# Kernel tuning notes

Hardware: AMD Instinct MI355X
Metric: run time of the kernel (lower is better)

The kernel has to match this reference:

```python
import jax, jax.numpy as jnp
import numpy as np

# ---- static config (matches init_kwargs) ----
R_MAX = 5.0
K_RBF = 32
F = 128            # features_dim
H = 4              # num_att_heads
DH = F // H        # 32
T = 3              # num_interactions
NG = 64            # num_graphs
INV_AVG = 1.0 / 16.0   # 1/avg_num_neighbors
NUM_ELEM = 10
DEG = [1, 3, 5, 7]     # (2l+1) for l=0..3
OFF = np.cumsum([0] + DEG)  # [0,1,4,9,16]
SH = 16

silu = jax.nn.silu


def sph_harm(v):
    """Real spherical harmonics l=0..3, normalized input, e3nn 'component' norm
    (sum_m Y_lm^2 = 2l+1 pointwise). v: [E,3] -> [E,16]."""
    r = jnp.linalg.norm(v, axis=-1, keepdims=True)
    u = v / jnp.maximum(r, 1e-9)
    x, y, z = u[..., 0], u[..., 1], u[..., 2]
    one = jnp.ones_like(x)
    s3, s5, s15 = np.sqrt(3.0), np.sqrt(5.0), np.sqrt(15.0)
    s70, s105, s42, s7 = np.sqrt(70.0), np.sqrt(105.0), np.sqrt(42.0), np.sqrt(7.0)
    z2 = z * z
    comps = [
        one,
        s3 * x, s3 * y, s3 * z,
        s15 * x * y, s15 * y * z, 0.5 * s5 * (3.0 * z2 - 1.0), s15 * x * z, 0.5 * s15 * (x * x - y * y),
        0.25 * s70 * y * (3.0 * x * x - y * y),
        s105 * x * y * z,
        0.25 * s42 * y * (5.0 * z2 - 1.0),
        0.5 * s7 * z * (5.0 * z2 - 3.0),
        0.25 * s42 * x * (5.0 * z2 - 1.0),
        0.5 * s105 * z * (x * x - y * y),
        0.25 * s70 * x * (x * x - 3.0 * y * y),
    ]
    return jnp.stack(comps, axis=-1)


def cosine_cutoff(r):
    return 0.5 * (jnp.cos(jnp.pi * r / R_MAX) + 1.0) * (r < R_MAX)


def gaussian_rbf(r):
    mu = jnp.linspace(0.0, R_MAX, K_RBF)
    gamma = (K_RBF / R_MAX) ** 2
    return jnp.exp(-gamma * (r[:, None] - mu[None, :]) ** 2)  # [E,K]


def deg_reduce(x):  # [...,16] -> [...,4] sum of components per degree
    return jnp.stack([x[..., OFF[l]:OFF[l + 1]].sum(-1) for l in range(4)], axis=-1)


def deg_expand(x):  # [...,4] -> [...,16] broadcast per-degree scalar to components
    return jnp.repeat(x, np.array(DEG), axis=-1, total_repeat_length=SH)


def setup_inputs() -> dict:
    key = jax.random.key(0)
    ks = jax.random.split(key, 32)
    N, E = 30000, 480000
    inp = {
        'positions': jax.random.normal(ks[0], (N, 3), jnp.float32),
        'species': jax.random.randint(ks[1], (N,), 0, NUM_ELEM, jnp.int32),
        'senders': jax.random.randint(ks[2], (E,), 0, N, jnp.int32),
        'receivers': jax.random.randint(ks[3], (E,), 0, N, jnp.int32),
        'batch': jnp.sort(jax.random.randint(ks[4], (N,), 0, NG, jnp.int32)),
    }
    def w(k, shape, fan_in):
        return jax.random.normal(k, shape, jnp.float32) / np.sqrt(fan_in)
    inp['embed'] = w(ks[5], (NUM_ELEM, F), 1)
    inp['Wq'] = w(ks[6], (T, F, F), F)
    inp['Wk'] = w(ks[7], (T, F, F), F)
    inp['Wv'] = w(ks[8], (T, F, F), F)
    inp['Wo'] = w(ks[9], (T, F, F), F)
    inp['Wrbf1'] = w(ks[10], (T, K_RBF, F), K_RBF)
    inp['brbf1'] = jnp.zeros((T, F), jnp.float32)
    inp['Wrbf2'] = w(ks[11], (T, F, F), F)
    inp['Wdeg'] = w(ks[12], (T, 4, F), 4)
    inp['Wq2'] = w(ks[13], (T, F, F), F)
    inp['Wk2'] = w(ks[14], (T, F, F), F)
    inp['Wex1'] = w(ks[15], (T, F + 4, F), F + 4)
    inp['bex1'] = jnp.zeros((T, F), jnp.float32)
    inp['Wex2'] = w(ks[16], (T, F, F + 4), F)
    inp['bex2'] = jnp.zeros((T, F + 4), jnp.float32)
    inp['Wo1'] = w(ks[17], (F, F), F)
    inp['bo1'] = jnp.zeros((F,), jnp.float32)
    inp['Wo2'] = w(ks[18], (F, 1), F)
    inp['bo2'] = jnp.zeros((1,), jnp.float32)
    return inp


def reference(positions, species, senders, receivers, batch, embed,
              Wq, Wk, Wv, Wo, Wrbf1, brbf1, Wrbf2, Wdeg, Wq2, Wk2,
              Wex1, bex1, Wex2, bex2, Wo1, bo1, Wo2, bo2):
    N = positions.shape[0]
    seg = lambda d, i: jax.ops.segment_sum(d, i, num_segments=N)
    # edge geometry
    vec = positions[receivers] - positions[senders]          # [E,3]
    r = jnp.linalg.norm(vec, axis=-1)                        # [E]
    Y = sph_harm(vec)                                        # [E,16]
    C = cosine_cutoff(r)                                     # [E]
    R = gaussian_rbf(r)                                      # [E,K]
    # embeddings
    f = embed[species]                                       # [N,F]
    ev = seg(Y * C[:, None], receivers) * INV_AVG            # [N,16]
    for t in range(T):
        # per-edge filter: radial MLP + degree-wise EV contraction
        w = silu(R @ Wrbf1[t] + brbf1[t]) @ Wrbf2[t]         # [E,F]
        dd = deg_reduce(ev[senders] * ev[receivers])         # [E,4]
        w = w + dd @ Wdeg[t]
        wH = w.reshape(-1, H, DH)                            # [E,H,DH]
        # invariant (feature) attention branch
        q = (f @ Wq[t]).reshape(-1, H, DH)
        k = (f @ Wk[t]).reshape(-1, H, DH)
        v = (f @ Wv[t]).reshape(-1, H, DH)
        alpha = (q[receivers] * wH * k[senders]).sum(-1) / np.sqrt(DH) * C[:, None]  # [E,H]
        agg = seg(alpha[:, :, None] * v[senders], receivers).reshape(-1, F) * INV_AVG
        f = f + agg @ Wo[t]
        # euclidean-variable (geometric) attention branch (4 heads <-> 4 degrees)
        q2 = (f @ Wq2[t]).reshape(-1, 4, DH)
        k2 = (f @ Wk2[t]).reshape(-1, 4, DH)
        a2 = (q2[receivers] * wH * k2[senders]).sum(-1) / np.sqrt(DH) * C[:, None]   # [E,4]
        ev = ev + seg(deg_expand(a2) * Y, receivers) * INV_AVG
        # exchange / interaction block (mix invariants with degree-wise EV norms)
        ev_inv = deg_reduce(ev * ev)                         # [N,4]
        h = jnp.concatenate([f, ev_inv], axis=-1)            # [N,F+4]
        yb = silu(h @ Wex1[t] + bex1[t]) @ Wex2[t] + bex2[t] # [N,F+4]
        f = f + yb[:, :F]
        ev = ev + deg_expand(yb[:, F:]) * ev
    node_e = silu(f @ Wo1 + bo1) @ Wo2 + bo2                 # [N,1]
    energy = jax.ops.segment_sum(node_e[:, 0], batch, num_segments=NG)  # [NG]
    return energy
```

## Files before the change

kernel.cpp:

```cpp
#include <hip/hip_runtime.h>
#include <math.h>

#define F 128
#define KRBF 32
#define TINTER 3
#define RMAX 5.0f
#define INV_AVG (1.0f/16.0f)
#define GAMMA 40.96f
#define RSQRT_DH 0.17677669529663689f
#define PI_F 3.14159265358979323846f
#define TAB_N 2048
#define APITCH 68
#define SCB 256

__device__ __forceinline__ float silu_f(float x) { return x / (1.0f + expf(-x)); }
__device__ __forceinline__ int deg_of(int c) { return (c == 0) ? 0 : (c < 4) ? 1 : (c < 9) ? 2 : 3; }

__device__ __forceinline__ unsigned int pk_bf2(float lo, float hi) {
    unsigned int a = __float_as_uint(lo), b = __float_as_uint(hi);
    unsigned int ar = (a + 0x7fffu + ((a >> 16) & 1u)) >> 16;
    unsigned int br = (b + 0x7fffu + ((b >> 16) & 1u)) >> 16;
    return ar | (br << 16);
}
__device__ __forceinline__ float up_lo(unsigned int u) { return __uint_as_float(u << 16); }
// ... 60 lines not shown
        __syncthreads();
        s[tid] += t;
        __syncthreads();
    }
    if (tid < nb) boff[tid] = s[tid] - v;
    if (tid == 1023) off[N] = s[1023];
}

__global__ void scan_add_kernel(int* __restrict__ off, int* __restrict__ cur,
                                const int* __restrict__ boff, int N)
{
    int i = blockIdx.x * blockDim.x + threadIdx.x;
    if (i < N) {
        int v = off[i] + boff[i / SCB];
        off[i] = v; cur[i] = v;
    }
}

__global__ void scatter_kernel(const int* __restrict__ rcv, int* __restrict__ cur,
                               int* __restrict__ elist, int E)
{
    int e = blockIdx.x * blockDim.x + threadIdx.x;
    if (e < E) {
        int p = atomicAdd(&cur[rcv[e]], 1);
        elist[p] = e;
    }
}

__global__ void edge_geom_csr_kernel(const int* __restrict__ elist,
                                     const float* __restrict__ pos,
                                     const int* __restrict__ snd,
                                     const int* __restrict__ rcv,
                                     int* __restrict__ sp, int* __restrict__ rcvp,
                                     float2* __restrict__ rcC,
                                     float* __restrict__ Yp, int E)
{
    int ei = blockIdx.x * blockDim.x + threadIdx.x;
    if (ei >= E) return;
    int e = elist[ei];
    int s = snd[e], rc = rcv[e];
    sp[ei] = s; rcvp[ei] = rc;
    float vx = pos[rc * 3 + 0] - pos[s * 3 + 0];
    float vy = pos[rc * 3 + 1] - pos[s * 3 + 1];
    float vz = pos[rc * 3 + 2] - pos[s * 3 + 2];
    float r = sqrtf(vx * vx + vy * vy + vz * vz);
    float rinv = 1.0f / fmaxf(r, 1e-9f);
    float x = vx * rinv, y = vy * rinv, z = vz * rinv;
    float x2 = x * x, y2 = y * y, z2 = z * z;
    const float s3 = 1.7320508075688772f, s5 = 2.23606797749979f, s15 = 3.872983346207417f;
    const float s70 = 8.366600265340756f, s105 = 10.246950765959598f;
    const float s42 = 6.48074069840786f, s7 = 2.6457513110645907f;
    float Y[16];
    Y[0] = 1.0f;
    Y[1] = s3 * x; Y[2] = s3 * y; Y[3] = s3 * z;
    Y[4] = s15 * x * y; Y[5] = s15 * y * z; Y[6] = 0.5f * s5 * (3.0f * z2 - 1.0f);
    Y[7] = s15 * x * z; Y[8] = 0.5f * s15 * (x2 - y2);
    Y[9]  = 0.25f * s70 * y * (3.0f * x2 - y2);
    Y[10] = s105 * x * y * z;
    Y[11] = 0.25f * s42 * y * (5.0f * z2 - 1.0f);
    Y[12] = 0.5f * s7 * z * (5.0f * z2 - 3.0f);
    Y[13] = 0.25f * s42 * x * (5.0f * z2 - 1.0f);
    Y[14] = 0.5f * s105 * z * (x2 - y2);
    Y[15] = 0.25f * s70 * x * (x2 - 3.0f * y2);
    float C = (r < RMAX) ? 0.5f * (cosf(PI_F * r / RMAX) + 1.0f) : 0.0f;
    rcC[ei] = make_float2(r, C);
    #pragma unroll
    for (int c = 0; c < 16; c++) Yp[(size_t)ei * 16 + c] = Y[c];
}

__global__ void ev0_kernel(const int* __restrict__ off,
                           const float* __restrict__ Yp, const float2* __restrict__ rcC,
                           float* __restrict__ ev, int N)
{
    int n = blockIdx.x * 16 + (threadIdx.x >> 4);
    int c = threadIdx.x & 15;
    if (n >= N) return;
    float acc = 0.0f;
    int e0 = off[n], e1 = off[n + 1];
    for (int ei = e0; ei < e1; ei++)
        acc += Yp[(size_t)ei * 16 + c] * rcC[ei].y;
    ev[n * 16 + c] = acc * INV_AVG;
}

__global__ void embed_kernel(const int* __restrict__ species,
                             const float* __restrict__ embed,
                             float* __restrict__ f, int N)
{
    int n = blockIdx.x;
    if (n >= N) return;
    int j = threadIdx.x;
    f[n * F + j] = embed[species[n] * F + j];
}

__global__ void pack_w_kernel(const float* __restrict__ Wq, const float* __restrict__ Wk,
                              const float* __restrict__ Wv, const float* __restrict__ Wo,
                              const float* __restrict__ Wq2, const float* __restrict__ Wk2,
                              unsigned int* __restrict__ Wpk)
{
    int tid = blockIdx.x * blockDim.x + threadIdx.x;
    if (tid >= 18 * 8192) return;
    int mat = tid >> 13;
    int rem = tid & 8191;
    int iw = rem & 3;
    int n = (rem >> 2) & 15;
    int quad = (rem >> 6) & 3;
    int kb = (rem >> 8) & 3;
    int ct = rem >> 10;
    const float* fam = (mat < 3) ? Wq : (mat < 6) ? Wk : (mat < 9) ? Wv
                     : (mat < 12) ? Wo : (mat < 15) ? Wq2 : Wk2;
    const float* src = fam + (size_t)(mat % 3) * F * F;
    int k = kb * 32 + quad * 8 + iw * 2;
    int col = ct * 16 + n;
    Wpk[tid] = pk_bf2(src[k * F + col], src[(k + 1) * F + col]);
// ... 34 lines not shown
    float r = idx * (RMAX / (TAB_N - 1));
    __shared__ float sR[4][KRBF];
    __shared__ float sH[4][F];
    if (lane < KRBF) {
        float mu = lane * (RMAX / (KRBF - 1));
        float d = r - mu;
        sR[wave][lane] = expf(-GAMMA * d * d);
    }
    __syncthreads();
    float h0 = b1[lane], h1 = b1[lane + 64];
    #pragma unroll
    for (int kk = 0; kk < KRBF; kk++) {
        float rv = sR[wave][kk];
        h0 += rv * W1[kk * F + lane];
        h1 += rv * W1[kk * F + lane + 64];
    }
    sH[wave][lane] = silu_f(h0);
    sH[wave][lane + 64] = silu_f(h1);
    __syncthreads();
    float w0 = 0.0f, w1 = 0.0f;
    for (int i = 0; i < F; i++) {
        float hv = sH[wave][i];
        w0 += hv * W2[i * F + 2 * lane];
        w1 += hv * W2[i * F + 2 * lane + 1];
    }
    unsigned int w = pk_bf2(w0, w1);
    size_t base = ((size_t)t * TAB_N + idx) * 64 + lane;
    tab2w[base * 2] = w;
    if (idx > 0) tab2w[(base - 64) * 2 + 1] = w;
    if (idx == TAB_N - 1) tab2w[base * 2 + 1] = w;
}

__global__ void dd_kernel(const int* __restrict__ sp, const int* __restrict__ rcvp,
                          const float* __restrict__ ev, float4* __restrict__ ddl, int E)
{
    int ei = blockIdx.x * blockDim.x + threadIdx.x;
    if (ei >= E) return;
    int s = sp[ei], rc = rcvp[ei];
    const float4* a = (const float4*)(ev + (size_t)s * 16);
    const float4* b = (const float4*)(ev + (size_t)rc * 16);
    float4 a0 = a[0], a1 = a[1], a2 = a[2], a3 = a[3];
    float4 b0 = b[0], b1 = b[1], b2 = b[2], b3 = b[3];
    float d0 = a0.x * b0.x;
    float d1 = a0.y * b0.y + a0.z * b0.z + a0.w * b0.w;
    float d2 = a1.x * b1.x + a1.y * b1.y + a1.z * b1.z + a1.w * b1.w + a2.x * b2.x;
    float d3 = a2.y * b2.y + a2.z * b2.z + a2.w * b2.w
             + a3.x * b3.x + a3.y * b3.y + a3.z * b3.z + a3.w * b3.w;
    ddl[ei] = make_float4(d0, d1, d2, d3);
}

__global__ __launch_bounds__(256) void node_gemm_mfma_kernel(
    const float* __restrict__ A,
    const unsigned int* __restrict__ B0, const unsigned int* __restrict__ B1,
    const unsigned int* __restrict__ B2,
    float* __restrict__ out0, unsigned int* __restrict__ out1, unsigned int* __restrict__ out2,
    int N, int nw, int accumulate, int ileave)
{
    __shared__ unsigned int sA[64 * APITCH];
    int tid = threadIdx.x;
    int n0 = blockIdx.x * 64;
    #pragma unroll
    for (int rep = 0; rep < 16; rep++) {
        int idx = rep * 256 + tid;
        int node = idx >> 6, jj = idx & 63;
        int n = n0 + node;
        float2 v = (n < N) ? ((const float2*)A)[(size_t)n * 64 + jj] : make_float2(0.f, 0.f);
        sA[node * APITCH + jj] = pk_bf2(v.x, v.y);
    }
    __syncthreads();
    int wave = tid >> 6, lane = tid & 63;
    int quad = lane >> 4, col = lane & 15;
    int mrow = wave * 16 + col;
    s16x8 af[4];
    #pragma unroll
    for (int kb = 0; kb < 4; kb++) {
        FragU fu;
        fu.u = *(const uint4*)&sA[mrow * APITCH + kb * 16 + quad * 4];
        af[kb] = fu.s;
    }
    for (int m = 0; m < nw; m++) {
        const unsigned int* B = (m == 0) ? B0 : (m == 1) ? B1 : B2;
        for (int ct = 0; ct < 8; ct++) {
            f32x4 acc = {0.f, 0.f, 0.f, 0.f};
            #pragma unroll
            for (int kb = 0; kb < 4; kb++) {
                FragU bu;
                bu.u = *(const uint4*)&B[(size_t)((ct * 16 + kb * 4 + quad) * 16 + col) * 4];
                acc = __builtin_amdgcn_mfma_f32_16x16x32_bf16(af[kb], bu.s, acc, 0, 0, 0);
            }
            if (m == 0) {
                #pragma unroll
                for (int r = 0; r < 4; r++) {
                    int n = n0 + wave * 16 + quad * 4 + r;
                    if (n < N) {
                        size_t ix = (size_t)n * F + ct * 16 + col;
                        out0[ix] = accumulate ? out0[ix] + acc[r] : acc[r];
                    }
                }
            } else {
                unsigned int* o16 = (m == 1) ? out1 : out2;
                #pragma unroll
                for (int r = 0; r < 4; r++) {
                    float other = __shfl_xor(acc[r], 1, 64);
                    if (!(lane & 1)) {
                        int n = n0 + wave * 16 + quad * 4 + r;
                        if (n < N) {
                            size_t base = (size_t)n * 64 + ct * 8 + (col >> 1);
                            if (ileave)
                                out1[base * 2 + (m - 1)] = pk_bf2(acc[r], other);
                            else
                                o16[base] = pk_bf2(acc[r], other);
                        }
                    }
                }
            }
        }
    }
}

__global__ __launch_bounds__(256) void fused_o_qk_kernel(
    const float* __restrict__ agg,
    const unsigned int* __restrict__ Bo, const unsigned int* __restrict__ Bq2,
    const unsigned int* __restrict__ Bk2,
    float* __restrict__ f, float* __restrict__ qout, unsigned int* __restrict__ k16p,
    int N)
{
    __shared__ unsigned int sA[64 * APITCH];
    int tid = threadIdx.x;
    int n0 = blockIdx.x * 64;
    #pragma unroll
    for (int rep = 0; rep < 16; rep++) {
        int idx = rep * 256 + tid;
        int node = idx >> 6, jj = idx & 63;
        int n = n0 + node;
        float2 v = (n < N) ? ((const float2*)agg)[(size_t)n * 64 + jj] : make_float2(0.f, 0.f);
        sA[node * APITCH + jj] = pk_bf2(v.x, v.y);
    }
    __syncthreads();
    int wave = tid >> 6, lane = tid & 63;
    int quad = lane >> 4, col = lane & 15;
    int mrow = wave * 16 + col;
    s16x8 af[4];
    #pragma unroll
    for (int kb = 0; kb < 4; kb++) {
// ... 55 lines not shown
            acc = __builtin_amdgcn_mfma_f32_16x16x32_bf16(a2[kb], bu.s, acc, 0, 0, 0);
        }
        #pragma unroll
        for (int r = 0; r < 4; r++) {
            float other = __shfl_xor(acc[r], 1, 64);
            if (!(lane & 1)) {
                int n = n0 + wave * 16 + quad * 4 + r;
                if (n < N) k16p[(size_t)n * 64 + ct * 8 + (col >> 1)] = pk_bf2(acc[r], other);
            }
        }
    }
}

__device__ __forceinline__ float edge_alpha(
    int lane, f32x2 qq, f32x2 wd0, f32x2 wd1, f32x2 wd2, f32x2 wd3,
    const uint2* __restrict__ tab2, float rr, float4 dd, unsigned int ku)
{
    float u = rr * ((float)(TAB_N - 1) / RMAX);
    int i0 = (int)u;
    i0 = (i0 > TAB_N - 2) ? (TAB_N - 2) : i0;
    float fr = u - (float)i0;
    int i0s = __builtin_amdgcn_readfirstlane(i0);
    uint2 tp = (tab2 + (size_t)i0s * 64)[lane];
    f32x2 a = up2(tp.x), b = up2(tp.y);
    f32x2 fr2 = {fr, fr};
    f32x2 w = a + fr2 * (b - a);
    f32x2 d0 = {dd.x, dd.x}, d1 = {dd.y, dd.y}, d2 = {dd.z, dd.z}, d3 = {dd.w, dd.w};
    w = w + d0 * wd0 + d1 * wd1 + d2 * wd2 + d3 * wd3;
    f32x2 p2 = qq * w * up2(ku);
    return red16_dpp(p2.x + p2.y);
}

__global__ __launch_bounds__(256) void edge_pass_node_kernel(
    const int* __restrict__ off, const int* __restrict__ sp,
    const float2* __restrict__ rcC, const float4* __restrict__ ddl,
    const float* __restrict__ Yp,
    const float* __restrict__ qbuf,
    const uint2* __restrict__ kv16, const unsigned int* __restrict__ k16p,
    const uint2* __restrict__ tab2, const float* __restrict__ Wdeg_t,
    float* __restrict__ outbuf, int N, int mode)
{
    int wave = threadIdx.x >> 6;
    int lane = threadIdx.x & 63;
    int n = blockIdx.x * 4 + wave;
    if (n >= N) return;

    const float2* wdp = (const float2*)Wdeg_t;
    float2 w0f = wdp[lane], w1f = wdp[64 + lane], w2f = wdp[128 + lane], w3f = wdp[192 + lane];
    f32x2 wd0 = {w0f.x, w0f.y}, wd1 = {w1f.x, w1f.y};
    f32x2 wd2 = {w2f.x, w2f.y}, wd3 = {w3f.x, w3f.y};

    int e0 = __builtin_amdgcn_readfirstlane(off[n]);
    int e1 = __builtin_amdgcn_readfirstlane(off[n + 1]);
    float2 qf = ((const float2*)qbuf)[(size_t)n * 64 + lane];
    const float QS = RSQRT_DH * INV_AVG;
    f32x2 qq = {qf.x * QS, qf.y * QS};
    f32x2 acc2 = {0.f, 0.f};
    float devacc = 0.0f;

    int ei = e0;
    if (mode == 0) {
        for (; ei + 3 < e1; ei += 4) {
            int sA = sp[ei], sB = sp[ei + 1], sC = sp[ei + 2], sD = sp[ei + 3];
            float2 rcA = rcC[ei], rcB = rcC[ei + 1], rcCc = rcC[ei + 2], rcD = rcC[ei + 3];
            float4 ddA = ddl[ei], ddB = ddl[ei + 1], ddC = ddl[ei + 2], ddD = ddl[ei + 3];
            uint2 kvA = kv16[(size_t)sA * 64 + lane];
            uint2 kvB = kv16[(size_t)sB * 64 + lane];
            uint2 kvC = kv16[(size_t)sC * 64 + lane];
            uint2 kvD = kv16[(size_t)sD * 64 + lane];
            float alA = rcA.y * edge_alpha(lane, qq, wd0, wd1, wd2, wd3, tab2, rcA.x, ddA, kvA.x);
            float alB = rcB.y * edge_alpha(lane, qq, wd0, wd1, wd2, wd3, tab2, rcB.x, ddB, kvB.x);
            float alC = rcCc.y * edge_alpha(lane, qq, wd0, wd1, wd2, wd3, tab2, rcCc.x, ddC, kvC.x);
            float alD = rcD.y * edge_alpha(lane, qq, wd0, wd1, wd2, wd3, tab2, rcD.x, ddD, kvD.x);
            f32x2 vA = {alA, alA}, vB = {alB, alB}, vC = {alC, alC}, vD = {alD, alD};
            acc2 = acc2 + vA * up2(kvA.y) + vB * up2(kvB.y)
                        + vC * up2(kvC.y) + vD * up2(kvD.y);
        }
        for (; ei < e1; ei++) {
            int sA = sp[ei];
            float2 rcA = rcC[ei];
            uint2 kvA = kv16[(size_t)sA * 64 + lane];
            float alA = rcA.y * edge_alpha(lane, qq, wd0, wd1, wd2, wd3, tab2, rcA.x, ddl[ei], kvA.x);
            f32x2 vA = {alA, alA};
            acc2 = acc2 + vA * up2(kvA.y);
        }
        ((float2*)outbuf)[(size_t)n * 64 + lane] = make_float2(acc2.x, acc2.y);
    } else {
        int c = lane & 15;
        int g = lane >> 4;
        int ssel = ((c == 0) ? 0 : (c < 4) ? 16 : (c < 9) ? 32 : 48) + c;
        for (; ei + 3 < e1; ei += 4) {
            int sA = sp[ei], sB = sp[ei + 1], sC = sp[ei + 2], sD = sp[ei + 3];
            float2 rcA = rcC[ei], rcB = rcC[ei + 1], rcCc = rcC[ei + 2], rcD = rcC[ei + 3];
            float4 ddA = ddl[ei], ddB = ddl[ei + 1], ddC = ddl[ei + 2], ddD = ddl[ei + 3];
            unsigned int kA = k16p[(size_t)sA * 64 + lane];
            unsigned int kB = k16p[(size_t)sB * 64 + lane];
            unsigned int kC = k16p[(size_t)sC * 64 + lane];
            unsigned int kD = k16p[(size_t)sD * 64 + lane];
            float alA = rcA.y * edge_alpha(lane, qq, wd0, wd1, wd2, wd3, tab2, rcA.x, ddA, kA);
            float alB = rcB.y * edge_alpha(lane, qq, wd0, wd1, wd2, wd3, tab2, rcB.x, ddB, kB);
            float alC = rcCc.y * edge_alpha(lane, qq, wd0, wd1, wd2, wd3, tab2, rcCc.x, ddC, kC);
            float alD = rcD.y * edge_alpha(lane, qq, wd0, wd1, wd2, wd3, tab2, rcD.x, ddD, kD);
            float adA = __shfl(alA, ssel);
            float adB = __shfl(alB, ssel);
            float adC = __shfl(alC, ssel);
            float adD = __shfl(alD, ssel);
            float ad = (g == 0) ? adA : (g == 1) ? adB : (g == 2) ? adC : adD;
            devacc += ad * Yp[(size_t)(ei + g) * 16 + c];
        }
        for (; ei < e1; ei++) {
            int sA = sp[ei];
            float2 rcA = rcC[ei];
            unsigned int kA = k16p[(size_t)sA * 64 + lane];
            float alA = rcA.y * edge_alpha(lane, qq, wd0, wd1, wd2, wd3, tab2, rcA.x, ddl[ei], kA);
            float adA = __shfl(alA, ssel);
            if (g == 0) devacc += adA * Yp[(size_t)ei * 16 + c];
        }
        devacc += __shfl_xor(devacc, 16, 64);
        devacc += __shfl_xor(devacc, 32, 64);
        if (lane < 16) outbuf[n * 16 + lane] = devacc;
    }
}

__global__ __launch_bounds__(256) void exchange_mfma_kernel(
    float* __restrict__ f, float* __restrict__ ev, const float* __restrict__ dEv,
    const unsigned int* __restrict__ B1, const float* __restrict__ Wex1,
    const float* __restrict__ bex1,
    const unsigned int* __restrict__ B2, const float* __restrict__ Wex2,
    const float* __restrict__ bex2, int N)
{
    __shared__ unsigned int sA[64 * APITCH];
    __shared__ float sev[64][17];
    __shared__ float sEvInv[64][4];
    __shared__ float sW1x[4][F];
    __shared__ float sW2x[F][4];
    __shared__ float sB1[F];
    __shared__ float sB2[F];
    __shared__ float sb2x[4];
    __shared__ float syb[64][4];

    int tid = threadIdx.x;
    int n0 = blockIdx.x * 64;
    #pragma unroll
    for (int rep = 0; rep < 16; rep++) {
        int idx = rep * 256 + tid;
        int node = idx >> 6, jj = idx & 63;
        int n = n0 + node;
        float2 v = (n < N) ? ((const float2*)f)[(size_t)n * 64 + jj] : make_float2(0.f, 0.f);
        sA[node * APITCH + jj] = pk_bf2(v.x, v.y);
    }
    for (int idx = tid; idx < 64 * 16; idx += 256) {
        int node = idx >> 4, c = idx & 15;
        int n = n0 + node;
        sev[node][c] = (n < N) ? (ev[(size_t)n * 16 + c] + dEv[(size_t)n * 16 + c]) : 0.0f;
    }
    for (int idx = tid; idx < 4 * F; idx += 256)
        sW1x[idx >> 7][idx & 127] = Wex1[(size_t)(128 + (idx >> 7)) * F + (idx & 127)];
    for (int idx = tid; idx < F * 4; idx += 256)
        sW2x[idx >> 2][idx & 3] = Wex2[(size_t)(idx >> 2) * (F + 4) + 128 + (idx & 3)];
    if (tid < F) sB1[tid] = bex1[tid];
    else sB2[tid - F] = bex2[tid - F];
    if (tid < 4) sb2x[tid] = bex2[F + tid];
    __syncthreads();
    {
        int node = tid >> 2, d = tid & 3;
        int c0 = (d == 0) ? 0 : (d == 1) ? 1 : (d == 2) ? 4 : 9;
        int c1 = (d == 0) ? 1 : (d == 1) ? 4 : (d == 2) ? 9 : 16;
        float a = 0.0f;
        for (int c = c0; c < c1; c++) { float v = sev[node][c]; a += v * v; }
        sEvInv[node][d] = a;
    }
    int wave = tid >> 6, lane = tid & 63;
    int quad = lane >> 4, col = lane & 15;
    int mrow = wave * 16 + col;
    s16x8 af[4];
    #pragma unroll
    for (int kb = 0; kb < 4; kb++) {
        FragU fu;
        fu.u = *(const uint4*)&sA[mrow * APITCH + kb * 16 + quad * 4];
        af[kb] = fu.s;
    }
    __syncthreads();
    float evq[4][4];
    #pragma unroll
    for (int r = 0; r < 4; r++) {
        int node = wave * 16 + quad * 4 + r;
        #pragma unroll
        for (int d = 0; d < 4; d++) evq[r][d] = sEvInv[node][d];
    }
    for (int ct = 0; ct < 8; ct++) {
        f32x4 acc = {0.f, 0.f, 0.f, 0.f};
        #pragma unroll
        for (int kb = 0; kb < 4; kb++) {
            FragU bu;
            bu.u = *(const uint4*)&B1[(size_t)((ct * 16 + kb * 4 + quad) * 16 + col) * 4];
// ... 1 lines not shown
        }
        int j = ct * 16 + col;
        float w0 = sW1x[0][j], w1 = sW1x[1][j], w2 = sW1x[2][j], w3 = sW1x[3][j];
        float bj = sB1[j];
        #pragma unroll
        for (int r = 0; r < 4; r++) {
            float x = acc[r] + bj + evq[r][0] * w0 + evq[r][1] * w1
                    + evq[r][2] * w2 + evq[r][3] * w3;
            float h = silu_f(x);
            float other = __shfl_xor(h, 1, 64);
            if (!(lane & 1)) {
                int node = wave * 16 + quad * 4 + r;
                sA[node * APITCH + ct * 8 + (col >> 1)] = pk_bf2(h, other);
            }
        }
    }
    __syncthreads();
    s16x8 a2[4];
    #pragma unroll
    for (int kb = 0; kb < 4; kb++) {
        FragU fu;
        fu.u = *(const uint4*)&sA[mrow * APITCH + kb * 16 + quad * 4];
        a2[kb] = fu.s;
    }
    {
        int node = tid >> 2, d = tid & 3;
        float a = sb2x[d];
        for (int dw = 0; dw < 64; dw++) {
            unsigned int u = sA[node * APITCH + dw];
            a += up_lo(u) * sW2x[2 * dw][d] + up_hi(u) * sW2x[2 * dw + 1][d];
        }
        syb[node][d] = a;
    }
    for (int ct = 0; ct < 8; ct++) {
        f32x4 acc = {0.f, 0.f, 0.f, 0.f};
        #pragma unroll
        for (int kb = 0; kb < 4; kb++) {
            FragU bu;
            bu.u = *(const uint4*)&B2[(size_t)((ct * 16 + kb * 4 + quad) * 16 + col) * 4];
            acc = __builtin_amdgcn_mfma_f32_16x16x32_bf16(a2[kb], bu.s, acc, 0, 0, 0);
        }
        int j = ct * 16 + col;
        float bj = sB2[j];
        #pragma unroll
        for (int r = 0; r < 4; r++) {
            int n = n0 + wave * 16 + quad * 4 + r;
            if (n < N) {
                size_t ix = (size_t)n * F + j;
                f[ix] = f[ix] + acc[r] + bj;
            }
        }
    }
    __syncthreads();
    for (int idx = tid; idx < 64 * 16; idx += 256) {
        int node = idx >> 4, c = idx & 15;
        int n = n0 + node;
        if (n < N) ev[(size_t)n * 16 + c] = sev[node][c] * (1.0f + syb[node][deg_of(c)]);
    }
}

__global__ __launch_bounds__(256) void readout_mfma_kernel(
    const float* __restrict__ f, const unsigned int* __restrict__ B,
    const float* __restrict__ bo1, const float* __restrict__ Wo2,
    const float* __restrict__ bo2, float* __restrict__ node_e, int N)
{
    __shared__ unsigned int sA[64 * APITCH];
    __shared__ float sB1[F];
    __shared__ float sW2[F];
    int tid = threadIdx.x;
    int n0 = blockIdx.x * 64;
    #pragma unroll
    for (int rep = 0; rep < 16; rep++) {
        int idx = rep * 256 + tid;
        int node = idx >> 6, jj = idx & 63;
        int n = n0 + node;
        float2 v = (n < N) ? ((const float2*)f)[(size_t)n * 64 + jj] : make_float2(0.f, 0.f);
        sA[node * APITCH + jj] = pk_bf2(v.x, v.y);
    }
    if (tid < F) sB1[tid] = bo1[tid];
    else sW2[tid - F] = Wo2[tid - F];
    __syncthreads();
    int wave = tid >> 6, lane = tid & 63;
    int quad = lane >> 4, col = lane & 15;
    int mrow = wave * 16 + col;
    s16x8 af[4];
    #pragma unroll
    for (int kb = 0; kb < 4; kb++) {
        FragU fu;
        fu.u = *(const uint4*)&sA[mrow * APITCH + kb * 16 + quad * 4];
        af[kb] = fu.s;
    }
    float part[4] = {0.f, 0.f, 0.f, 0.f};
    for (int ct = 0; ct < 8; ct++) {
        f32x4 acc = {0.f, 0.f, 0.f, 0.f};
        #pragma unroll
        for (int kb = 0; kb < 4; kb++) {
            FragU bu;
            bu.u = *(const uint4*)&B[(size_t)((ct * 16 + kb * 4 + quad) * 16 + col) * 4];
            acc = __builtin_amdgcn_mfma_f32_16x16x32_bf16(af[kb], bu.s, acc, 0, 0, 0);
        }
        int j = ct * 16 + col;
        float bj = sB1[j], wj = sW2[j];
        #pragma unroll
        for (int r = 0; r < 4; r++) part[r] += silu_f(acc[r] + bj) * wj;
    }
    #pragma unroll
    for (int r = 0; r < 4; r++) part[r] = red16_dpp(part[r]);
    if (col == 0) {
        #pragma unroll
        for (int r = 0; r < 4; r++) {
            int n = n0 + wave * 16 + quad * 4 + r;
            if (n < N) node_e[n] = part[r] + bo2[0];
        }
    }
}

__global__ __launch_bounds__(256) void energy_reduce_kernel(
    const float* __restrict__ node_e, const int* __restrict__ batch,
    float* __restrict__ energy, int N)
{
    __shared__ float eacc[64];
    if (threadIdx.x < 64) eacc[threadIdx.x] = 0.0f;
    __syncthreads();
    for (int n = blockIdx.x * blockDim.x + threadIdx.x; n < N; n += gridDim.x * blockDim.x)
        atomicAdd(&eacc[batch[n]], node_e[n]);
    __syncthreads();
    if (threadIdx.x < 64) atomicAdd(&energy[threadIdx.x], eacc[threadIdx.x]);
}

extern "C" void kernel_launch(void* const* d_in, const int* in_sizes, int n_in,
                              void* d_out, int out_size, void* d_ws, size_t ws_size,
                              hipStream_t stream)
{
    const float* positions = (const float*)d_in[0];
    const int*   species   = (const int*)d_in[1];
    const int*   senders   = (const int*)d_in[2];
    const int*   receivers = (const int*)d_in[3];
    const int*   batch     = (const int*)d_in[4];
    const float* embed     = (const float*)d_in[5];
    const float* Wq    = (const float*)d_in[6];
    const float* Wk    = (const float*)d_in[7];
    const float* Wv    = (const float*)d_in[8];
    const float* Wo    = (const float*)d_in[9];
    const float* Wrbf1 = (const float*)d_in[10];
    const float* brbf1 = (const float*)d_in[11];
    const float* Wrbf2 = (const float*)d_in[12];
    const float* Wdeg  = (const float*)d_in[13];
    const float* Wq2   = (const float*)d_in[14];
    const float* Wk2   = (const float*)d_in[15];
    const float* Wex1  = (const float*)d_in[16];
    const float* bex1  = (const float*)d_in[17];
    const float* Wex2  = (const float*)d_in[18];
    const float* bex2  = (const float*)d_in[19];
    const float* Wo1   = (const float*)d_in[20];
    const float* bo1   = (const float*)d_in[21];
    const float* Wo2   = (const float*)d_in[22];
    const float* bo2   = (const float*)d_in[23];

    int N = in_sizes[0] / 3;
    int E = in_sizes[2];

    float* ws     = (float*)d_ws;
    float* Yp     = ws;  ws += (size_t)E * 16;
    float2* rcC   = (float2*)ws; ws += (size_t)E * 2;
    float* f      = ws;  ws += (size_t)N * F;
    float* evb    = ws;  ws += (size_t)N * 16;
    float* dEv    = ws;  ws += (size_t)N * 16;
    float* q      = ws;  ws += (size_t)N * F;
    float* agg    = ws;  ws += (size_t)N * F;
    float* node_e = ws;  ws += (size_t)N;
    float* un     = ws;  ws += (size_t)E * 18;
    uint2* tab2 = (uint2*)un;
    uint2* kv16 = tab2 + (size_t)TINTER * TAB_N * 64;
    unsigned int* k16p = (unsigned int*)(kv16 + (size_t)N * 64);
    float4* ddl   = (float4*)(k16p + (size_t)N * 64);
    int* sp    = (int*)ws;  ws += E;
    int* rcvp  = (int*)ws;  ws += E;
    int* cnt   = (int*)ws;  ws += N;
    int* off   = (int*)ws;  ws += N + 1;
    int* cur   = (int*)ws;  ws += N;
    int* elist = (int*)ws;  ws += E;
    int* bsum  = (int*)ws;  ws += 1024;
    int* boff  = (int*)ws;  ws += 1024;
    unsigned int* Wpk  = (unsigned int*)ws;  ws += 18 * 8192;
    unsigned int* Wpk2 = (unsigned int*)ws;  ws += 7 * 8192;

    int nb = (N + SCB - 1) / SCB;
    hipMemsetAsync(cnt, 0, (size_t)N * sizeof(int), stream);
    count_kernel<<<(E + 255) / 256, 256, 0, stream>>>(receivers, cnt, E);
    scan_part_kernel<<<nb, SCB, 0, stream>>>(cnt, off, bsum, N);
    scan_mid_kernel<<<1, 1024, 0, stream>>>(bsum, boff, off, N, nb);
    scan_add_kernel<<<(N + 255) / 256, 256, 0, stream>>>(off, cur, boff, N);
    scatter_kernel<<<(E + 255) / 256, 256, 0, stream>>>(receivers, cur, elist, E);

    edge_geom_csr_kernel<<<(E + 255) / 256, 256, 0, stream>>>(elist, positions, senders,
                                                              receivers, sp, rcvp, rcC, Yp, E);
    pack_w_kernel<<<(18 * 8192 + 255) / 256, 256, 0, stream>>>(Wq, Wk, Wv, Wo, Wq2, Wk2, Wpk);
    pack_ex_kernel<<<(7 * 8192 + 255) / 256, 256, 0, stream>>>(Wex1, Wex2, Wo1, Wpk2);
    build_table_kernel<<<dim3(TAB_N / 4, TINTER), 256, 0, stream>>>(Wrbf1, brbf1, Wrbf2,
                                                                    (unsigned int*)tab2);
    ev0_kernel<<<(N + 15) / 16, 256, 0, stream>>>(off, Yp, rcC, evb, N);
    embed_kernel<<<N, F, 0, stream>>>(species, embed, f, N);

    int nmb = (N + 63) / 64;
    int npb = (N + 3) / 4;
    int edb = (E + 255) / 256;
    for (int t = 0; t < TINTER; t++) {
        const unsigned int* Wpk_q  = Wpk + (size_t)(0 * 3 + t) * 8192;
        const unsigned int* Wpk_k  = Wpk + (size_t)(1 * 3 + t) * 8192;
        const unsigned int* Wpk_v  = Wpk + (size_t)(2 * 3 + t) * 8192;
        const unsigned int* Wpk_o  = Wpk + (size_t)(3 * 3 + t) * 8192;
        const unsigned int* Wpk_q2 = Wpk + (size_t)(4 * 3 + t) * 8192;
        const unsigned int* Wpk_k2 = Wpk + (size_t)(5 * 3 + t) * 8192;
        const uint2* tab_t = tab2 + (size_t)t * TAB_N * 64;
        const float* Wdeg_t = Wdeg + (size_t)t * 4 * F;
        node_gemm_mfma_kernel<<<nmb, 256, 0, stream>>>(f, Wpk_q, Wpk_k, Wpk_v,
                                                       q, (unsigned int*)kv16, nullptr,
                                                       N, 3, 0, 1);
        dd_kernel<<<edb, 256, 0, stream>>>(sp, rcvp, evb, ddl, E);
        edge_pass_node_kernel<<<npb, 256, 0, stream>>>(off, sp, rcC, ddl, Yp,
            q, kv16, nullptr, tab_t, Wdeg_t, agg, N, 0);
        fused_o_qk_kernel<<<nmb, 256, 0, stream>>>(agg, Wpk_o, Wpk_q2, Wpk_k2,
                                                   f, q, k16p, N);
        edge_pass_node_kernel<<<npb, 256, 0, stream>>>(off, sp, rcC, ddl, Yp,
            q, nullptr, k16p, tab_t, Wdeg_t, dEv, N, 1);
        exchange_mfma_kernel<<<nmb, 256, 0, stream>>>(f, evb, dEv,
            Wpk2 + (size_t)t * 8192, Wex1 + (size_t)t * (F + 4) * F, bex1 + (size_t)t * F,
            Wpk2 + (size_t)(3 + t) * 8192, Wex2 + (size_t)t * F * (F + 4),
            bex2 + (size_t)t * (F + 4), N);
    }
    readout_mfma_kernel<<<nmb, 256, 0, stream>>>(f, Wpk2 + (size_t)6 * 8192,
                                                 bo1, Wo2, bo2, node_e, N);
    hipMemsetAsync(d_out, 0, (size_t)out_size * sizeof(float), stream);
    energy_reduce_kernel<<<16, 256, 0, stream>>>(node_e, batch, (float*)d_out, N);
}
```

Baseline: 796.9 us.

## Fuse next-layer QKV and readout into exchange kernel; pack edge data

Moves the Q/K/V projection for the next interaction, and the final readout MLP, into the epilogue of the exchange kernel. The updated bf16 features are reused from shared memory, which removes a separate launch and a re-read of f per layer. Per-edge sender index, r, cutoff and degree dot-products are interleaved into one float4-pair array, so the edge pass does contiguous loads instead of three separate streams. The agg buffer is aliased onto q, which now serves as both input and output of the edge pass and the o-projection kernel. That aliasing is a correctness risk if the node-level reads and writes overlap.

Measured after the change: 775.1 us. -2.7%, faster.

```diff
diff --git a/kernel.cpp b/kernel.cpp
--- a/kernel.cpp
+++ b/kernel.cpp
@@ -116,7 +116,8 @@
                                      const int* __restrict__ snd,
                                      const int* __restrict__ rcv,
                                      int* __restrict__ sp, int* __restrict__ rcvp,
-                                     float2* __restrict__ rcC,
+                                     float* __restrict__ Cb,
+                                     float4* __restrict__ edata,
                                      float* __restrict__ Yp, int E)
 {
     int ei = blockIdx.x * blockDim.x + threadIdx.x;
@@ -147,13 +148,14 @@
     Y[14] = 0.5f * s105 * z * (x2 - y2);
     Y[15] = 0.25f * s70 * x * (x2 - 3.0f * y2);
     float C = (r < RMAX) ? 0.5f * (cosf(PI_F * r / RMAX) + 1.0f) : 0.0f;
-    rcC[ei] = make_float2(r, C);
+    Cb[ei] = C;
+    edata[2 * ei] = make_float4(__int_as_float(s), r, C, 0.0f);
     #pragma unroll
     for (int c = 0; c < 16; c++) Yp[(size_t)ei * 16 + c] = Y[c];
 }
 
 __global__ void ev0_kernel(const int* __restrict__ off,
-                           const float* __restrict__ Yp, const float2* __restrict__ rcC,
+                           const float* __restrict__ Yp, const float* __restrict__ Cb,
                            float* __restrict__ ev, int N)
 {
     int n = blockIdx.x * 16 + (threadIdx.x >> 4);
@@ -162,7 +164,7 @@
     float acc = 0.0f;
     int e0 = off[n], e1 = off[n + 1];
     for (int ei = e0; ei < e1; ei++)
-        acc += Yp[(size_t)ei * 16 + c] * rcC[ei].y;
+        acc += Yp[(size_t)ei * 16 + c] * Cb[ei];
     ev[n * 16 + c] = acc * INV_AVG;
 }
 
@@ -263,7 +265,7 @@
 }
 
 __global__ void dd_kernel(const int* __restrict__ sp, const int* __restrict__ rcvp,
-                          const float* __restrict__ ev, float4* __restrict__ ddl, int E)
+                          const float* __restrict__ ev, float4* __restrict__ edata, int E)
 {
     int ei = blockIdx.x * blockDim.x + threadIdx.x;
     if (ei >= E) return;
@@ -277,15 +279,15 @@
     float d2 = a1.x * b1.x + a1.y * b1.y + a1.z * b1.z + a1.w * b1.w + a2.x * b2.x;
     float d3 = a2.y * b2.y + a2.z * b2.z + a2.w * b2.w
              + a3.x * b3.x + a3.y * b3.y + a3.z * b3.z + a3.w * b3.w;
-    ddl[ei] = make_float4(d0, d1, d2, d3);
+    edata[2 * ei + 1] = make_float4(d0, d1, d2, d3);
 }
 
 __global__ __launch_bounds__(256) void node_gemm_mfma_kernel(
     const float* __restrict__ A,
     const unsigned int* __restrict__ B0, const unsigned int* __restrict__ B1,
     const unsigned int* __restrict__ B2,
-    float* __restrict__ out0, unsigned int* __restrict__ out1, unsigned int* __restrict__ out2,
-    int N, int nw, int accumulate, int ileave)
+    float* __restrict__ out0, unsigned int* __restrict__ out1,
+    int N)
 {
     __shared__ unsigned int sA[64 * APITCH];
     int tid = threadIdx.x;
@@ -309,7 +311,7 @@
         fu.u = *(const uint4*)&sA[mrow * APITCH + kb * 16 + quad * 4];
         af[kb] = fu.s;
     }
-    for (int m = 0; m < nw; m++) {
+    for (int m = 0; m < 3; m++) {
         const unsigned int* B = (m == 0) ? B0 : (m == 1) ? B1 : B2;
         for (int ct = 0; ct < 8; ct++) {
             f32x4 acc = {0.f, 0.f, 0.f, 0.f};
@@ -323,13 +325,9 @@
                 #pragma unroll
                 for (int r = 0; r < 4; r++) {
                     int n = n0 + wave * 16 + quad * 4 + r;
-                    if (n < N) {
-                        size_t ix = (size_t)n * F + ct * 16 + col;
-                        out0[ix] = accumulate ? out0[ix] + acc[r] : acc[r];
-                    }
+                    if (n < N) out0[(size_t)n * F + ct * 16 + col] = acc[r];
                 }
             } else {
-                unsigned int* o16 = (m == 1) ? out1 : out2;
                 #pragma unroll
                 for (int r = 0; r < 4; r++) {
                     float other = __shfl_xor(acc[r], 1, 64);
@@ -337,10 +335,7 @@
                         int n = n0 + wave * 16 + quad * 4 + r;
                         if (n < N) {
                             size_t base = (size_t)n * 64 + ct * 8 + (col >> 1);
-                            if (ileave)
-                                out1[base * 2 + (m - 1)] = pk_bf2(acc[r], other);
-                            else
-                                o16[base] = pk_bf2(acc[r], other);
+                            out1[base * 2 + (m - 1)] = pk_bf2(acc[r], other);
                         }
                     }
                 }
@@ -462,8 +457,7 @@
 }
 
 __global__ __launch_bounds__(256) void edge_pass_node_kernel(
-    const int* __restrict__ off, const int* __restrict__ sp,
-    const float2* __restrict__ rcC, const float4* __restrict__ ddl,
+    const int* __restrict__ off, const float4* __restrict__ edata,
     const float* __restrict__ Yp,
     const float* __restrict__ qbuf,
     const uint2* __restrict__ kv16, const unsigned int* __restrict__ k16p,
@@ -491,26 +485,29 @@
     int ei = e0;
     if (mode == 0) {
         for (; ei + 3 < e1; ei += 4) {
-            int sA = sp[ei], sB = sp[ei + 1], sC = sp[ei + 2], sD = sp[ei + 3];
-            float2 rcA = rcC[ei], rcB = rcC[ei + 1], rcCc = rcC[ei + 2], rcD = rcC[ei + 3];
-            float4 ddA = ddl[ei], ddB = ddl[ei + 1], ddC = ddl[ei + 2], ddD = ddl[ei + 3];
+            float4 hA = edata[2 * ei],     dA = edata[2 * ei + 1];
+            float4 hB = edata[2 * ei + 2], dB = edata[2 * ei + 3];
+            float4 hC = edata[2 * ei + 4], dC = edata[2 * ei + 5];
+            float4 hD = edata[2 * ei + 6], dD = edata[2 * ei + 7];
+            int sA = __float_as_int(hA.x), sB = __float_as_int(hB.x);
+            int sC = __float_as_int(hC.x), sD = __float_as_int(hD.x);
             uint2 kvA = kv16[(size_t)sA * 64 + lane];
             uint2 kvB = kv16[(size_t)sB * 64 + lane];
             uint2 kvC = kv16[(size_t)sC * 64 + lane];
             uint2 kvD = kv16[(size_t)sD * 64 + lane];
-            float alA = rcA.y * edge_alpha(lane, qq, wd0, wd1, wd2, wd3, tab2, rcA.x, ddA, kvA.x);
-            float alB = rcB.y * edge_alpha(lane, qq, wd0, wd1, wd2, wd3, tab2, rcB.x, ddB, kvB.x);
-            float alC = rcCc.y * edge_alpha(lane, qq, wd0, wd1, wd2, wd3, tab2, rcCc.x, ddC, kvC.x);
-            float alD = rcD.y * edge_alpha(lane, qq, wd0, wd1, wd2, wd3, tab2, rcD.x, ddD, kvD.x);
+            float alA = hA.z * edge_alpha(lane, qq, wd0, wd1, wd2, wd3, tab2, hA.y, dA, kvA.x);
+            float alB = hB.z * edge_alpha(lane, qq, wd0, wd1, wd2, wd3, tab2, hB.y, dB, kvB.x);
+            float alC = hC.z * edge_alpha(lane, qq, wd0, wd1, wd2, wd3, tab2, hC.y, dC, kvC.x);
+            float alD = hD.z * edge_alpha(lane, qq, wd0, wd1, wd2, wd3, tab2, hD.y, dD, kvD.x);
             f32x2 vA = {alA, alA}, vB = {alB, alB}, vC = {alC, alC}, vD = {alD, alD};
             acc2 = acc2 + vA * up2(kvA.y) + vB * up2(kvB.y)
                         + vC * up2(kvC.y) + vD * up2(kvD.y);
         }
         for (; ei < e1; ei++) {
-            int sA = sp[ei];
-            float2 rcA = rcC[ei];
+            float4 hA = edata[2 * ei], dA = edata[2 * ei + 1];
+            int sA = __float_as_int(hA.x);
             uint2 kvA = kv16[(size_t)sA * 64 + lane];
-            float alA = rcA.y * edge_alpha(lane, qq, wd0, wd1, wd2, wd3, tab2, rcA.x, ddl[ei], kvA.x);
+            float alA = hA.z * edge_alpha(lane, qq, wd0, wd1, wd2, wd3, tab2, hA.y, dA, kvA.x);
             f32x2 vA = {alA, alA};
             acc2 = acc2 + vA * up2(kvA.y);
         }
@@ -520,17 +517,20 @@
         int g = lane >> 4;
         int ssel = ((c == 0) ? 0 : (c < 4) ? 16 : (c < 9) ? 32 : 48) + c;
         for (; ei + 3 < e1; ei += 4) {
-            int sA = sp[ei], sB = sp[ei + 1], sC = sp[ei + 2], sD = sp[ei + 3];
-            float2 rcA = rcC[ei], rcB = rcC[ei + 1], rcCc = rcC[ei + 2], rcD = rcC[ei + 3];
-            float4 ddA = ddl[ei], ddB = ddl[ei + 1], ddC = ddl[ei + 2], ddD = ddl[ei + 3];
+            float4 hA = edata[2 * ei],     dA = edata[2 * ei + 1];
+            float4 hB = edata[2 * ei + 2], dB = edata[2 * ei + 3];
+            float4 hC = edata[2 * ei + 4], dC = edata[2 * ei + 5];
+            float4 hD = edata[2 * ei + 6], dD = edata[2 * ei + 7];
+            int sA = __float_as_int(hA.x), sB = __float_as_int(hB.x);
+            int sC = __float_as_int(hC.x), sD = __float_as_int(hD.x);
             unsigned int kA = k16p[(size_t)sA * 64 + lane];
             unsigned int kB = k16p[(size_t)sB * 64 + lane];
             unsigned int kC = k16p[(size_t)sC * 64 + lane];
             unsigned int kD = k16p[(size_t)sD * 64 + lane];
-            float alA = rcA.y * edge_alpha(lane, qq, wd0, wd1, wd2, wd3, tab2, rcA.x, ddA, kA);
-            float alB = rcB.y * edge_alpha(lane, qq, wd0, wd1, wd2, wd3, tab2, rcB.x, ddB, kB);
-            float alC = rcCc.y * edge_alpha(lane, qq, wd0, wd1, wd2, wd3, tab2, rcCc.x, ddC, kC);
-            float alD = rcD.y * edge_alpha(lane, qq, wd0, wd1, wd2, wd3, tab2, rcD.x, ddD, kD);
+            float alA = hA.z * edge_alpha(lane, qq, wd0, wd1, wd2, wd3, tab2, hA.y, dA, kA);
+            float alB = hB.z * edge_alpha(lane, qq, wd0, wd1, wd2, wd3, tab2, hB.y, dB, kB);
+            float alC = hC.z * edge_alpha(lane, qq, wd0, wd1, wd2, wd3, tab2, hC.y, dC, kC);
+            float alD = hD.z * edge_alpha(lane, qq, wd0, wd1, wd2, wd3, tab2, hD.y, dD, kD);
             float adA = __shfl(alA, ssel);
             float adB = __shfl(alB, ssel);
             float adC = __shfl(alC, ssel);
@@ -539,10 +539,10 @@
             devacc += ad * Yp[(size_t)(ei + g) * 16 + c];
         }
         for (; ei < e1; ei++) {
-            int sA = sp[ei];
-            float2 rcA = rcC[ei];
+            float4 hA = edata[2 * ei], dA = edata[2 * ei + 1];
+            int sA = __float_as_int(hA.x);
             unsigned int kA = k16p[(size_t)sA * 64 + lane];
-            float alA = rcA.y * edge_alpha(lane, qq, wd0, wd1, wd2, wd3, tab2, rcA.x, ddl[ei], kA);
+            float alA = hA.z * edge_alpha(lane, qq, wd0, wd1, wd2, wd3, tab2, hA.y, dA, kA);
             float adA = __shfl(alA, ssel);
             if (g == 0) devacc += adA * Yp[(size_t)ei * 16 + c];
         }
@@ -552,12 +552,18 @@
     }
 }
 
-__global__ __launch_bounds__(256) void exchange_mfma_kernel(
+__global__ __launch_bounds__(256) void exchange_fused_kernel(
     float* __restrict__ f, float* __restrict__ ev, const float* __restrict__ dEv,
     const unsigned int* __restrict__ B1, const float* __restrict__ Wex1,
     const float* __restrict__ bex1,
     const unsigned int* __restrict__ B2, const float* __restrict__ Wex2,
-    const float* __restrict__ bex2, int N)
+    const float* __restrict__ bex2,
+    const unsigned int* __restrict__ Bq, const unsigned int* __restrict__ Bk,
+    const unsigned int* __restrict__ Bv,
+    float* __restrict__ qout, unsigned int* __restrict__ kvout,
+    const float* __restrict__ bo1, const float* __restrict__ Wo2,
+    const float* __restrict__ bo2, float* __restrict__ node_e,
+    int last, int N)
 {
     __shared__ unsigned int sA[64 * APITCH];
     __shared__ float sev[64][17];
@@ -568,6 +574,8 @@
     __shared__ float sB2[F];
     __shared__ float sb2x[4];
     __shared__ float syb[64][4];
+    __shared__ float sRB[F];
+    __shared__ float sRW[F];
 
     int tid = threadIdx.x;
     int n0 = blockIdx.x * 64;
@@ -591,6 +599,10 @@
     if (tid < F) sB1[tid] = bex1[tid];
     else sB2[tid - F] = bex2[tid - F];
     if (tid < 4) sb2x[tid] = bex2[F + tid];
+    if (last) {
+        if (tid < F) sRB[tid] = bo1[tid];
+        else sRW[tid - F] = Wo2[tid - F];
+    }
     __syncthreads();
     {
         int node = tid >> 2, d = tid & 3;
@@ -658,6 +670,7 @@
         }
         syb[node][d] = a;
     }
+    __syncthreads();
     for (int ct = 0; ct < 8; ct++) {
         f32x4 acc = {0.f, 0.f, 0.f, 0.f};
         #pragma unroll
@@ -670,11 +683,16 @@
         float bj = sB2[j];
         #pragma unroll
         for (int r = 0; r < 4; r++) {
-            int n = n0 + wave * 16 + quad * 4 + r;
+            int node = wave * 16 + quad * 4 + r;
+            int n = n0 + node;
+            float fx = 0.0f;
             if (n < N) {
                 size_t ix = (size_t)n * F + j;
-                f[ix] = f[ix] + acc[r] + bj;
-            }
+                fx = f[ix] + acc[r] + bj;
+                f[ix] = fx;
+            }
+            float other = __shfl_xor(fx, 1, 64);
+            if (!(lane & 1)) sA[node * APITCH + ct * 8 + (col >> 1)] = pk_bf2(fx, other);
         }
     }
     __syncthreads();
@@ -683,60 +701,74 @@
         int n = n0 + node;
         if (n < N) ev[(size_t)n * 16 + c] = sev[node][c] * (1.0f + syb[node][deg_of(c)]);
     }
-}
-
-__global__ __launch_bounds__(256) void readout_mfma_kernel(
-    const float* __restrict__ f, const unsigned int* __restrict__ B,
-    const float* __restrict__ bo1, const float* __restrict__ Wo2,
-    const float* __restrict__ bo2, float* __restrict__ node_e, int N)
-{
-    __shared__ unsigned int sA[64 * APITCH];
-    __shared__ float sB1[F];
-    __shared__ float sW2[F];
-    int tid = threadIdx.x;
-    int n0 = blockIdx.x * 64;
-    #pragma unroll
-    for (int rep = 0; rep < 16; rep++) {
-        int idx = rep * 256 + tid;
-        int node = idx >> 6, jj = idx & 63;
-        int n = n0 + node;
-        float2 v = (n < N) ? ((const float2*)f)[(size_t)n * 64 + jj] : make_float2(0.f, 0.f);
-        sA[node * APITCH + jj] = pk_bf2(v.x, v.y);
-    }
-    if (tid < F) sB1[tid] = bo1[tid];
-    else sW2[tid - F] = Wo2[tid - F];
-    __syncthreads();
-    int wave = tid >> 6, lane = tid & 63;
-    int quad = lane >> 4, col = lane & 15;
-    int mrow = wave * 16 + col;
-    s16x8 af[4];
+    s16x8 a3[4];
     #pragma unroll
     for (int kb = 0; kb < 4; kb++) {
         FragU fu;
         fu.u = *(const uint4*)&sA[mrow * APITCH + kb * 16 + quad * 4];
-        af[kb] = fu.s;
-    }
-    float part[4] = {0.f, 0.f, 0.f, 0.f};
-    for (int ct = 0; ct < 8; ct++) {
-        f32x4 acc = {0.f, 0.f, 0.f, 0.f};
-        #pragma unroll
-        for (int kb = 0; kb < 4; kb++) {
-            FragU bu;
-            bu.u = *(const uint4*)&B[(size_t)((ct * 16 + kb * 4 + quad) * 16 + col) * 4];
-            acc = __builtin_amdgcn_mfma_f32_16x16x32_bf16(af[kb], bu.s, acc, 0, 0, 0);
-        }
-        int j = ct * 16 + col;
-        float bj = sB1[j], wj = sW2[j];
-        #pragma unroll
-        for (int r = 0; r < 4; r++) part[r] += silu_f(acc[r] + bj) * wj;
-    }
-    #pragma unroll
-    for (int r = 0; r < 4; r++) part[r] = red16_dpp(part[r]);
-    if (col == 0) {
-        #pragma unroll
-        for (int r = 0; r < 4; r++) {
-            int n = n0 + wave * 16 + quad * 4 + r;
-            if (n < N) node_e[n] = part[r] + bo2[0];
+        a3[kb] = fu.s;
+    }
+    if (!last) {
+        for (int ct = 0; ct < 8; ct++) {
+            f32x4 acc = {0.f, 0.f, 0.f, 0.f};
+            #pragma unroll
+            for (int kb = 0; kb < 4; kb++) {
+                FragU bu;
+                bu.u = *(const uint4*)&Bq[(size_t)((ct * 16 + kb * 4 + quad) * 16 + col) * 4];
+                acc = __builtin_amdgcn_mfma_f32_16x16x32_bf16(a3[kb], bu.s, acc, 0, 0, 0);
+            }
+            #pragma unroll
+            for (int r = 0; r < 4; r++) {
+                int n = n0 + wave * 16 + quad * 4 + r;
+                if (n < N) qout[(size_t)n * F + ct * 16 + col] = acc[r];
+            }
+        }
+        for (int m = 0; m < 2; m++) {
+            const unsigned int* B = (m == 0) ? Bk : Bv;
+            for (int ct = 0; ct < 8; ct++) {
+                f32x4 acc = {0.f, 0.f, 0.f, 0.f};
+                #pragma unroll
+                for (int kb = 0; kb < 4; kb++) {
+                    FragU bu;
+                    bu.u = *(const uint4*)&B[(size_t)((ct * 16 + kb * 4 + quad) * 16 + col) * 4];
+                    acc = __builtin_amdgcn_mfma_f32_16x16x32_bf16(a3[kb], bu.s, acc, 0, 0, 0);
+                }
+                #pragma unroll
+                for (int r = 0; r < 4; r++) {
+                    float other = __shfl_xor(acc[r], 1, 64);
+                    if (!(lane & 1)) {
+                        int n = n0 + wave * 16 + quad * 4 + r;
+                        if (n < N) {
+                            size_t base = (size_t)n * 64 + ct * 8 + (col >> 1);
+                            kvout[base * 2 + m] = pk_bf2(acc[r], other);
+                        }
+                    }
+                }
+            }
+        }
+    } else {
+        float part[4] = {0.f, 0.f, 0.f, 0.f};
+        for (int ct = 0; ct < 8; ct++) {
+            f32x4 acc = {0.f, 0.f, 0.f, 0.f};
+            #pragma unroll
+            for (int kb = 0; kb < 4; kb++) {
+                FragU bu;
+                bu.u = *(const uint4*)&Bq[(size_t)((ct * 16 + kb * 4 + quad) * 16 + col) * 4];
+                acc = __builtin_amdgcn_mfma_f32_16x16x32_bf16(a3[kb], bu.s, acc, 0, 0, 0);
+            }
+            int j = ct * 16 + col;
+            float bj = sRB[j], wj = sRW[j];
+            #pragma unroll
+            for (int r = 0; r < 4; r++) part[r] += silu_f(acc[r] + bj) * wj;
+        }
+        #pragma unroll
+        for (int r = 0; r < 4; r++) part[r] = red16_dpp(part[r]);
+        if (col == 0) {
+            #pragma unroll
+            for (int r = 0; r < 4; r++) {
+                int n = n0 + wave * 16 + quad * 4 + r;
+                if (n < N) node_e[n] = part[r] + bo2[0];
+            }
         }
     }
 }
@@ -788,18 +820,16 @@
 
     float* ws     = (float*)d_ws;
     float* Yp     = ws;  ws += (size_t)E * 16;
-    float2* rcC   = (float2*)ws; ws += (size_t)E * 2;
+    float4* edata = (float4*)ws; ws += (size_t)E * 8;
     float* f      = ws;  ws += (size_t)N * F;
     float* evb    = ws;  ws += (size_t)N * 16;
     float* dEv    = ws;  ws += (size_t)N * 16;
     float* q      = ws;  ws += (size_t)N * F;
-    float* agg    = ws;  ws += (size_t)N * F;
     float* node_e = ws;  ws += (size_t)N;
-    float* un     = ws;  ws += (size_t)E * 18;
-    uint2* tab2 = (uint2*)un;
-    uint2* kv16 = tab2 + (size_t)TINTER * TAB_N * 64;
-    unsigned int* k16p = (unsigned int*)(kv16 + (size_t)N * 64);
-    float4* ddl   = (float4*)(k16p + (size_t)N * 64);
+    float* Cb     = ws;  ws += (size_t)E;
+    uint2* tab2 = (uint2*)ws;  ws += (size_t)TINTER * TAB_N * 64 * 2;
+    uint2* kv16 = (uint2*)ws;  ws += (size_t)N * 64 * 2;
+    unsigned int* k16p = (unsigned int*)ws;  ws += (size_t)N * 64;
     int* sp    = (int*)ws;  ws += E;
     int* rcvp  = (int*)ws;  ws += E;
     int* cnt   = (int*)ws;  ws += N;
@@ -820,43 +850,46 @@
     scatter_kernel<<<(E + 255) / 256, 256, 0, stream>>>(receivers, cur, elist, E);
 
     edge_geom_csr_kernel<<<(E + 255) / 256, 256, 0, stream>>>(elist, positions, senders,
-                                                              receivers, sp, rcvp, rcC, Yp, E);
+                                                              receivers, sp, rcvp, Cb,
+                                                              edata, Yp, E);
     pack_w_kernel<<<(18 * 8192 + 255) / 256, 256, 0, stream>>>(Wq, Wk, Wv, Wo, Wq2, Wk2, Wpk);
     pack_ex_kernel<<<(7 * 8192 + 255) / 256, 256, 0, stream>>>(Wex1, Wex2, Wo1, Wpk2);
     build_table_kernel<<<dim3(TAB_N / 4, TINTER), 256, 0, stream>>>(Wrbf1, brbf1, Wrbf2,
                                                                     (unsigned int*)tab2);
-    ev0_kernel<<<(N + 15) / 16, 256, 0, stream>>>(off, Yp, rcC, evb, N);
+    ev0_kernel<<<(N + 15) / 16, 256, 0, stream>>>(off, Yp, Cb, evb, N);
     embed_kernel<<<N, F, 0, stream>>>(species, embed, f, N);
 
     int nmb = (N + 63) / 64;
     int npb = (N + 3) / 4;
     int edb = (E + 255) / 256;
+    node_gemm_mfma_kernel<<<nmb, 256, 0, stream>>>(f, Wpk + 0 * 8192, Wpk + 3 * 8192,
+                                                   Wpk + 6 * 8192, q, (unsigned int*)kv16, N);
     for (int t = 0; t < TINTER; t++) {
-        const unsigned int* Wpk_q  = Wpk + (size_t)(0 * 3 + t) * 8192;
-        const unsigned int* Wpk_k  = Wpk + (size_t)(1 * 3 + t) * 8192;
-        const unsigned int* Wpk_v  = Wpk + (size_t)(2 * 3 + t) * 8192;
         const unsigned int* Wpk_o  = Wpk + (size_t)(3 * 3 + t) * 8192;
         const unsigned int* Wpk_q2 = Wpk + (size_t)(4 * 3 + t) * 8192;
         const unsigned int* Wpk_k2 = Wpk + (size_t)(5 * 3 + t) * 8192;
         const uint2* tab_t = tab2 + (size_t)t * TAB_N * 64;
         const float* Wdeg_t = Wdeg + (size_t)t * 4 * F;
-        node_gemm_mfma_kernel<<<nmb, 256, 0, stream>>>(f, Wpk_q, Wpk_k, Wpk_v,
-                                                       q, (unsigned int*)kv16, nullptr,
-                                                       N, 3, 0, 1);
-        dd_kernel<<<edb, 256, 0, stream>>>(sp, rcvp, evb, ddl, E);
-        edge_pass_node_kernel<<<npb, 256, 0, stream>>>(off, sp, rcC, ddl, Yp,
-            q, kv16, nullptr, tab_t, Wdeg_t, agg, N, 0);
-        fused_o_qk_kernel<<<nmb, 256, 0, stream>>>(agg, Wpk_o, Wpk_q2, Wpk_k2,
+        int last = (t == TINTER - 1);
+        const unsigned int* Bq_n = last ? (Wpk2 + (size_t)6 * 8192)
+                                        : (Wpk + (size_t)(0 * 3 + t + 1) * 8192);
+        const unsigned int* Bk_n = Wpk + (size_t)(1 * 3 + (last ? t : t + 1)) * 8192;
+        const unsigned int* Bv_n = Wpk + (size_t)(2 * 3 + (last ? t : t + 1)) * 8192;
+
+        dd_kernel<<<edb, 256, 0, stream>>>(sp, rcvp, evb, edata, E);
+        edge_pass_node_kernel<<<npb, 256, 0, stream>>>(off, edata, Yp,
+            q, kv16, nullptr, tab_t, Wdeg_t, q , N, 0);
+        fused_o_qk_kernel<<<nmb, 256, 0, stream>>>(q, Wpk_o, Wpk_q2, Wpk_k2,
                                                    f, q, k16p, N);
-        edge_pass_node_kernel<<<npb, 256, 0, stream>>>(off, sp, rcC, ddl, Yp,
+        edge_pass_node_kernel<<<npb, 256, 0, stream>>>(off, edata, Yp,
             q, nullptr, k16p, tab_t, Wdeg_t, dEv, N, 1);
-        exchange_mfma_kernel<<<nmb, 256, 0, stream>>>(f, evb, dEv,
+        exchange_fused_kernel<<<nmb, 256, 0, stream>>>(f, evb, dEv,
             Wpk2 + (size_t)t * 8192, Wex1 + (size_t)t * (F + 4) * F, bex1 + (size_t)t * F,
             Wpk2 + (size_t)(3 + t) * 8192, Wex2 + (size_t)t * F * (F + 4),
-            bex2 + (size_t)t * (F + 4), N);
-    }
-    readout_mfma_kernel<<<nmb, 256, 0, stream>>>(f, Wpk2 + (size_t)6 * 8192,
-                                                 bo1, Wo2, bo2, node_e, N);
+            bex2 + (size_t)t * (F + 4),
+            Bq_n, Bk_n, Bv_n, q, (unsigned int*)kv16,
+            bo1, Wo2, bo2, node_e, last, N);
+    }
     hipMemsetAsync(d_out, 0, (size_t)out_size * sizeof(float), stream);
     energy_reduce_kernel<<<16, 256, 0, stream>>>(node_e, batch, (float*)d_out, N);
 }
```
